# Optimization experiments

Measured on AMD Instinct MI355X. Metric: run time of the kernel, lower is better.

## Reference

```python
import jax, jax.numpy as jnp
import numpy as np
from jax import lax

THRESHOLD = 1.0  # threshold_potential from __init__
STRIDE = (1, 1)
PADDING = 'SAME'


def setup_inputs() -> dict:
    key = jax.random.key(0)
    k1, k2, k3 = jax.random.split(key, 3)
    input_to_layer = jax.random.normal(k1, (1, 512, 512, 16), dtype=jnp.float32)
    weights = jax.random.normal(k2, (3, 3, 16, 64), dtype=jnp.float32)
    old_potentials = jax.random.normal(k3, (1, 512, 512, 64), dtype=jnp.float32)
    return {
        'input_to_layer': input_to_layer,
        'weights': weights,
        'old_potentials': old_potentials,
    }


def reference(input_to_layer, weights, old_potentials):
    # conv2d NHWC x HWIO -> NHWC, SAME padding, stride 1 (as tf.nn.conv2d)
    out_conv = lax.conv_general_dilated(
        input_to_layer, weights,
        window_strides=STRIDE, padding=PADDING,
        dimension_numbers=('NHWC', 'HWIO', 'NHWC'))
    # accumulate membrane potential, fused threshold -> spike + reset
    new_potentials = out_conv + old_potentials
    spiked = new_potentials >= THRESHOLD
    curr_spikes = spiked.astype(new_potentials.dtype)
    new_potentials = jnp.where(spiked, 0.0, new_potentials)
    # original returns spikes; new_potentials is the updated state
    return curr_spikes, new_potentials
```

## Files before the change

kernel.cpp:

```cpp
#include <hip/hip_runtime.h>


#define H 512
#define W 512
#define CI 16
#define CO 64
#define TX 32
#define TY 8
#define XT 34
#define YT 10
#define PIX_US 24
#define KS 152

typedef float v4f __attribute__((ext_vector_type(4)));
typedef float f32x4 __attribute__((ext_vector_type(4)));
typedef short short8 __attribute__((ext_vector_type(8)));
typedef unsigned int uint4v __attribute__((ext_vector_type(4)));

__device__ __forceinline__ unsigned int pack2bf(float f0, float f1) {
    unsigned u0 = __builtin_bit_cast(unsigned, f0);
    unsigned u1 = __builtin_bit_cast(unsigned, f1);
    u0 = (u0 + 0x7FFFu + ((u0 >> 16) & 1u)) >> 16;
    u1 = (u1 + 0x7FFFu + ((u1 >> 16) & 1u)) >> 16;
    return u0 | (u1 << 16);
}

__global__ __launch_bounds__(256, 3)
void snn_conv_mfma(const float* __restrict__ in,
                   const float* __restrict__ w,
                   const float* __restrict__ oldp,
                   float* __restrict__ out_spk,
                   float* __restrict__ out_pot)
{
    __shared__ unsigned short s_in[YT * XT * PIX_US];
    __shared__ unsigned short s_w[CO * KS];

    const int tid = threadIdx.x;
    const int bx = blockIdx.x & 15;
    const int by = blockIdx.x >> 4;
    const int tx0 = bx * TX, ty0 = by * TY;

    {
        const int n  = tid & 63;
        const int kq = tid >> 6;
        #pragma unroll
        for (int kk = 0; kk < 18; ++kk) {
            const int k = kq * 36 + kk * 2;
            const float f0 = w[k * CO + n];
            const float f1 = w[(k + 1) * CO + n];
            *(unsigned int*)&s_w[n * KS + k] = pack2bf(f0, f1);
        }
    }

    for (int idx = tid; idx < YT * XT; idx += 256) {
        const int ly = idx / XT, lx = idx - ly * XT;
        const int gy = ty0 + ly - 1, gx = tx0 + lx - 1;
        uint4v pk0, pk1;
        if ((unsigned)gy < H && (unsigned)gx < W) {
            const v4f* p = (const v4f*)(in + (gy * W + gx) * CI);
            v4f a = p[0], b = p[1], c = p[2], d = p[3];
            pk0 = (uint4v){pack2bf(a.x, a.y), pack2bf(a.z, a.w),
                           pack2bf(b.x, b.y), pack2bf(b.z, b.w)};
            pk1 = (uint4v){pack2bf(c.x, c.y), pack2bf(c.z, c.w),
                           pack2bf(d.x, d.y), pack2bf(d.z, d.w)};
        } else {
            pk0 = (uint4v)0u;
            pk1 = (uint4v)0u;
        }
        uint4v* dst = (uint4v*)&s_in[idx * PIX_US];
        dst[0] = pk0;
        dst[1] = pk1;
    }
    __syncthreads();

    const int lane = tid & 63;
    const int wv   = tid >> 6;
    const int r    = lane & 15;
    const int quad = lane >> 4;
    const int half = quad & 1;
    const int tsel = quad >> 1;

    f32x4 acc[4][4] = {};

    int abase[4];
    #pragma unroll
    for (int mt = 0; mt < 4; ++mt) {
        const int rl = 2 * wv + (mt >> 1);
        const int xl = (mt & 1) * 16 + r;
        abase[mt] = (rl * XT + xl) * PIX_US + half * 8;
    }

    const short8 zero8 = {0, 0, 0, 0, 0, 0, 0, 0};

    #pragma unroll
    for (int ks5 = 0; ks5 < 5; ++ks5) {
        const int t0 = ks5 * 2;
        const int t1 = (ks5 == 4) ? 8 : ks5 * 2 + 1;
        const int off0 = ((t0 / 3) * XT + (t0 % 3)) * PIX_US;
        const int off1 = ((t1 / 3) * XT + (t1 % 3)) * PIX_US;
        const int aoff = tsel ? off1 : off0;
        const int koff = (ks5 < 4) ? (ks5 * 32 + quad * 8) : (128 + half * 8);

        short8 bf[4];
        #pragma unroll
        for (int nt = 0; nt < 4; ++nt)
            bf[nt] = *(const short8*)&s_w[(nt * 16 + r) * KS + koff];

        short8 af[4];
        #pragma unroll
        for (int mt = 0; mt < 4; ++mt) {
            short8 a = *(const short8*)&s_in[abase[mt] + aoff];
            if (ks5 == 4) a = (quad >= 2) ? zero8 : a;
            af[mt] = a;
        }

        #pragma unroll
        for (int mt = 0; mt < 4; ++mt)
            #pragma unroll
            for (int nt = 0; nt < 4; ++nt)
                acc[mt][nt] = __builtin_amdgcn_mfma_f32_16x16x32_bf16(
                    bf[nt], af[mt], acc[mt][nt], 0, 0, 0);
    }

    f32x4 oldv[4][4];
    int ebase[4];
    #pragma unroll
    for (int mt = 0; mt < 4; ++mt) {
        const int gy = ty0 + 2 * wv + (mt >> 1);
        const int gx = tx0 + (mt & 1) * 16 + r;
        ebase[mt] = (gy * W + gx) * CO + quad * 4;
        #pragma unroll
        for (int nt = 0; nt < 4; ++nt)
            oldv[mt][nt] = *(const f32x4*)(oldp + ebase[mt] + nt * 16);
    }

    #pragma unroll
    for (int mt = 0; mt < 4; ++mt) {
        #pragma unroll
        for (int nt = 0; nt < 4; ++nt) {
            const int idx = ebase[mt] + nt * 16;
            f32x4 np = acc[mt][nt] + oldv[mt][nt];
            f32x4 spk, pot;
            #pragma unroll
            for (int j = 0; j < 4; ++j) {
                const bool s = np[j] >= 1.0f;
                spk[j] = s ? 1.0f : 0.0f;
                pot[j] = s ? 0.0f : np[j];
            }
            *(f32x4*)(out_spk + idx) = spk;
            *(f32x4*)(out_pot + idx) = pot;
        }
    }
}

extern "C" void kernel_launch(void* const* d_in, const int* in_sizes, int n_in,
                              void* d_out, int out_size, void* d_ws, size_t ws_size,
                              hipStream_t stream) {
    const float* in   = (const float*)d_in[0];
    const float* w    = (const float*)d_in[1];
    const float* oldp = (const float*)d_in[2];
    float* out_spk = (float*)d_out;
    float* out_pot = out_spk + (size_t)H * W * CO;

    const int grid = (W / TX) * (H / TY);
    snn_conv_mfma<<<grid, 256, 0, stream>>>(in, w, oldp, out_spk, out_pot);
}
```

Measured before the change: 203.7 us.

## Prepack bf16 weights, halve tile height, prefetch old potentials, nontemporal stores

Weight packing to bf16 moves into a separate one-block kernel that writes to workspace, so each conv block just copies pre-packed 16-byte chunks into LDS. The tile height drops from 8 to 4 rows, halving per-wave accumulators and raising the occupancy hint to 4 blocks per CU, at the cost of more halo overhead per output. The old-potential loads are issued at kernel start so they overlap the LDS staging and MFMA work. Output stores become nontemporal to avoid polluting cache with streaming writes. The extra kernel launch adds a small fixed cost.

```diff
diff --git a/kernel.cpp b/kernel.cpp
--- a/kernel.cpp
+++ b/kernel.cpp
@@ -6,11 +6,12 @@
 #define CI 16
 #define CO 64
 #define TX 32
-#define TY 8
+#define TY 4
 #define XT 34
-#define YT 10
+#define YT 6
 #define PIX_US 24
 #define KS 152
+#define SW_CHUNKS ((CO * KS * 2) / 16)
 
 typedef float v4f __attribute__((ext_vector_type(4)));
 typedef float f32x4 __attribute__((ext_vector_type(4)));
@@ -25,35 +26,71 @@
     return u0 | (u1 << 16);
 }
 
-__global__ __launch_bounds__(256, 3)
+__global__ void snn_pack_w(const float* __restrict__ w,
+                           unsigned int* __restrict__ wsu)
+{
+    const int tid = threadIdx.x;
+    const int n  = tid & 63;
+    const int kq = tid >> 6;
+    #pragma unroll
+    for (int kk = 0; kk < 18; ++kk) {
+        const int k = kq * 36 + kk * 2;
+        const float f0 = w[k * CO + n];
+        const float f1 = w[(k + 1) * CO + n];
+        wsu[(n * KS + k) >> 1] = pack2bf(f0, f1);
+    }
+    if (kq == 3) {
+        #pragma unroll
+        for (int i = 0; i < 4; ++i)
+            wsu[((n * KS + 144) >> 1) + i] = 0u;
+    }
+}
+
+__global__ __launch_bounds__(256, 4)
 void snn_conv_mfma(const float* __restrict__ in,
-                   const float* __restrict__ w,
+                   const uint4v* __restrict__ wsv,
                    const float* __restrict__ oldp,
                    float* __restrict__ out_spk,
                    float* __restrict__ out_pot)
 {
     __shared__ unsigned short s_in[YT * XT * PIX_US];
-    __shared__ unsigned short s_w[CO * KS];
+    __shared__ alignas(16) unsigned short s_w[CO * KS];
 
     const int tid = threadIdx.x;
     const int bx = blockIdx.x & 15;
     const int by = blockIdx.x >> 4;
     const int tx0 = bx * TX, ty0 = by * TY;
 
+    const int lane = tid & 63;
+    const int wv   = tid >> 6;
+    const int r    = lane & 15;
+    const int quad = lane >> 4;
+    const int half = quad & 1;
+    const int tsel = quad >> 1;
+
+    f32x4 oldv[2][4];
+    int ebase[2];
+    #pragma unroll
+    for (int mt = 0; mt < 2; ++mt) {
+        const int gy = ty0 + wv;
+        const int gx = tx0 + mt * 16 + r;
+        ebase[mt] = (gy * W + gx) * CO + quad * 4;
+        #pragma unroll
+        for (int nt = 0; nt < 4; ++nt)
+            oldv[mt][nt] = *(const f32x4*)(oldp + ebase[mt] + nt * 16);
+    }
+
     {
-        const int n  = tid & 63;
-        const int kq = tid >> 6;
+        uint4v* dst = (uint4v*)s_w;
         #pragma unroll
-        for (int kk = 0; kk < 18; ++kk) {
-            const int k = kq * 36 + kk * 2;
-            const float f0 = w[k * CO + n];
-            const float f1 = w[(k + 1) * CO + n];
-            *(unsigned int*)&s_w[n * KS + k] = pack2bf(f0, f1);
+        for (int i = 0; i < 5; ++i) {
+            const int idx = tid + i * 256;
+            if (idx < SW_CHUNKS) dst[idx] = wsv[idx];
         }
     }
 
-    for (int idx = tid; idx < YT * XT; idx += 256) {
-        const int ly = idx / XT, lx = idx - ly * XT;
+    if (tid < YT * XT) {
+        const int ly = tid / XT, lx = tid - ly * XT;
         const int gy = ty0 + ly - 1, gx = tx0 + lx - 1;
         uint4v pk0, pk1;
         if ((unsigned)gy < H && (unsigned)gx < W) {
@@ -67,28 +104,18 @@
             pk0 = (uint4v)0u;
             pk1 = (uint4v)0u;
         }
-        uint4v* dst = (uint4v*)&s_in[idx * PIX_US];
+        uint4v* dst = (uint4v*)&s_in[tid * PIX_US];
         dst[0] = pk0;
         dst[1] = pk1;
     }
     __syncthreads();
 
-    const int lane = tid & 63;
-    const int wv   = tid >> 6;
-    const int r    = lane & 15;
-    const int quad = lane >> 4;
-    const int half = quad & 1;
-    const int tsel = quad >> 1;
+    f32x4 acc[2][4] = {};
 
-    f32x4 acc[4][4] = {};
-
-    int abase[4];
+    int abase[2];
     #pragma unroll
-    for (int mt = 0; mt < 4; ++mt) {
-        const int rl = 2 * wv + (mt >> 1);
-        const int xl = (mt & 1) * 16 + r;
-        abase[mt] = (rl * XT + xl) * PIX_US + half * 8;
-    }
+    for (int mt = 0; mt < 2; ++mt)
+        abase[mt] = (wv * XT + mt * 16 + r) * PIX_US + half * 8;
 
     const short8 zero8 = {0, 0, 0, 0, 0, 0, 0, 0};
 
@@ -106,36 +133,24 @@
         for (int nt = 0; nt < 4; ++nt)
             bf[nt] = *(const short8*)&s_w[(nt * 16 + r) * KS + koff];
 
-        short8 af[4];
+        short8 af[2];
         #pragma unroll
-        for (int mt = 0; mt < 4; ++mt) {
+        for (int mt = 0; mt < 2; ++mt) {
             short8 a = *(const short8*)&s_in[abase[mt] + aoff];
             if (ks5 == 4) a = (quad >= 2) ? zero8 : a;
             af[mt] = a;
         }
 
         #pragma unroll
-        for (int mt = 0; mt < 4; ++mt)
+        for (int mt = 0; mt < 2; ++mt)
             #pragma unroll
             for (int nt = 0; nt < 4; ++nt)
                 acc[mt][nt] = __builtin_amdgcn_mfma_f32_16x16x32_bf16(
                     bf[nt], af[mt], acc[mt][nt], 0, 0, 0);
     }
 
-    f32x4 oldv[4][4];
-    int ebase[4];
     #pragma unroll
-    for (int mt = 0; mt < 4; ++mt) {
-        const int gy = ty0 + 2 * wv + (mt >> 1);
-        const int gx = tx0 + (mt & 1) * 16 + r;
-        ebase[mt] = (gy * W + gx) * CO + quad * 4;
-        #pragma unroll
-        for (int nt = 0; nt < 4; ++nt)
-            oldv[mt][nt] = *(const f32x4*)(oldp + ebase[mt] + nt * 16);
-    }
-
-    #pragma unroll
-    for (int mt = 0; mt < 4; ++mt) {
+    for (int mt = 0; mt < 2; ++mt) {
         #pragma unroll
         for (int nt = 0; nt < 4; ++nt) {
             const int idx = ebase[mt] + nt * 16;
@@ -147,8 +162,8 @@
                 spk[j] = s ? 1.0f : 0.0f;
                 pot[j] = s ? 0.0f : np[j];
             }
-            *(f32x4*)(out_spk + idx) = spk;
-            *(f32x4*)(out_pot + idx) = pot;
+            __builtin_nontemporal_store(spk, (f32x4*)(out_spk + idx));
+            __builtin_nontemporal_store(pot, (f32x4*)(out_pot + idx));
         }
     }
 }
@@ -162,6 +177,9 @@
     float* out_spk = (float*)d_out;
     float* out_pot = out_spk + (size_t)H * W * CO;
 
+    snn_pack_w<<<1, 256, 0, stream>>>(w, (unsigned int*)d_ws);
+
     const int grid = (W / TX) * (H / TY);
-    snn_conv_mfma<<<grid, 256, 0, stream>>>(in, w, oldp, out_spk, out_pot);
+    snn_conv_mfma<<<grid, 256, 0, stream>>>(in, (const uint4v*)d_ws, oldp,
+                                            out_spk, out_pot);
 }
```

New measurement: 221.6 us. 1.09x slower.

## Split bf16 pre-conversion into setup kernel and read padded input from global

Applied to the files above, without the earlier changes.

A separate setup kernel converts the input to a zero-padded bf16 image and the weights to packed bf16 in workspace. The conv kernel drops shared memory and syncthreads, reading A and B fragments directly from global/L2 with smaller 16x4 pixel tiles per block and double-buffered weight loads. This removes per-block halo conversion and LDS staging, at the cost of an extra launch, an extra pass writing and reading the padded image, and more redundant global reads of neighbouring pixels and weights.

```diff
diff --git a/kernel.cpp b/kernel.cpp
--- a/kernel.cpp
+++ b/kernel.cpp
@@ -5,12 +5,11 @@
 #define W 512
 #define CI 16
 #define CO 64
-#define TX 32
-#define TY 8
-#define XT 34
-#define YT 10
-#define PIX_US 24
+#define PW 514
+#define PAD_PX (PW * PW)
 #define KS 152
+#define W_OFF_U16 0
+#define IN_OFF_U16 32768
 
 typedef float v4f __attribute__((ext_vector_type(4)));
 typedef float f32x4 __attribute__((ext_vector_type(4)));
@@ -25,22 +24,13 @@
     return u0 | (u1 << 16);
 }
 
-__global__ __launch_bounds__(256, 3)
-void snn_conv_mfma(const float* __restrict__ in,
-                   const float* __restrict__ w,
-                   const float* __restrict__ oldp,
-                   float* __restrict__ out_spk,
-                   float* __restrict__ out_pot)
+__global__ void snn_setup(const float* __restrict__ in,
+                          const float* __restrict__ w,
+                          unsigned short* __restrict__ ws)
 {
-    __shared__ unsigned short s_in[YT * XT * PIX_US];
-    __shared__ unsigned short s_w[CO * KS];
-
     const int tid = threadIdx.x;
-    const int bx = blockIdx.x & 15;
-    const int by = blockIdx.x >> 4;
-    const int tx0 = bx * TX, ty0 = by * TY;
-
-    {
+    if (blockIdx.x == gridDim.x - 1) {
+        unsigned int* wsu = (unsigned int*)(ws + W_OFF_U16);
         const int n  = tid & 63;
         const int kq = tid >> 6;
         #pragma unroll
@@ -48,31 +38,44 @@
             const int k = kq * 36 + kk * 2;
             const float f0 = w[k * CO + n];
             const float f1 = w[(k + 1) * CO + n];
-            *(unsigned int*)&s_w[n * KS + k] = pack2bf(f0, f1);
+            wsu[(n * KS + k) >> 1] = pack2bf(f0, f1);
         }
+        if (kq == 3) {
+            #pragma unroll
+            for (int i = 0; i < 4; ++i)
+                wsu[((n * KS + 144) >> 1) + i] = 0u;
+        }
+        return;
     }
+    const int p = blockIdx.x * 256 + tid;
+    if (p >= PAD_PX) return;
+    const int py = p / PW, px = p - py * PW;
+    uint4v pk0 = (uint4v)0u, pk1 = (uint4v)0u;
+    if (py >= 1 && py <= H && px >= 1 && px <= W) {
+        const v4f* q = (const v4f*)(in + ((py - 1) * W + (px - 1)) * CI);
+        v4f a = q[0], b = q[1], c = q[2], d = q[3];
+        pk0 = (uint4v){pack2bf(a.x, a.y), pack2bf(a.z, a.w),
+                       pack2bf(b.x, b.y), pack2bf(b.z, b.w)};
+        pk1 = (uint4v){pack2bf(c.x, c.y), pack2bf(c.z, c.w),
+                       pack2bf(d.x, d.y), pack2bf(d.z, d.w)};
+    }
+    uint4v* dst = (uint4v*)(ws + IN_OFF_U16 + p * CI);
+    dst[0] = pk0;
+    dst[1] = pk1;
+}
 
-    for (int idx = tid; idx < YT * XT; idx += 256) {
-        const int ly = idx / XT, lx = idx - ly * XT;
-        const int gy = ty0 + ly - 1, gx = tx0 + lx - 1;
-        uint4v pk0, pk1;
-        if ((unsigned)gy < H && (unsigned)gx < W) {
-            const v4f* p = (const v4f*)(in + (gy * W + gx) * CI);
-            v4f a = p[0], b = p[1], c = p[2], d = p[3];
-            pk0 = (uint4v){pack2bf(a.x, a.y), pack2bf(a.z, a.w),
-                           pack2bf(b.x, b.y), pack2bf(b.z, b.w)};
-            pk1 = (uint4v){pack2bf(c.x, c.y), pack2bf(c.z, c.w),
-                           pack2bf(d.x, d.y), pack2bf(d.z, d.w)};
-        } else {
-            pk0 = (uint4v)0u;
-            pk1 = (uint4v)0u;
-        }
-        uint4v* dst = (uint4v*)&s_in[idx * PIX_US];
-        dst[0] = pk0;
-        dst[1] = pk1;
-    }
-    __syncthreads();
+__global__ __launch_bounds__(256, 3)
+void snn_conv_mfma(const unsigned short* __restrict__ ws,
+                   const float* __restrict__ oldp,
+                   float* __restrict__ out_spk,
+                   float* __restrict__ out_pot)
+{
+    const unsigned short* pin = ws + IN_OFF_U16;
+    const unsigned short* wsb = ws + W_OFF_U16;
 
+    const int tid  = threadIdx.x;
+    const int bx   = blockIdx.x & 31;
+    const int by   = blockIdx.x >> 5;
     const int lane = tid & 63;
     const int wv   = tid >> 6;
     const int r    = lane & 15;
@@ -80,76 +83,64 @@
     const int half = quad & 1;
     const int tsel = quad >> 1;
 
-    f32x4 acc[4][4] = {};
+    const int gy = by * 4 + wv;
+    const int gx = bx * 16 + r;
 
-    int abase[4];
+    const int eb = (gy * W + gx) * CO + quad * 4;
+    f32x4 oldv[4];
     #pragma unroll
-    for (int mt = 0; mt < 4; ++mt) {
-        const int rl = 2 * wv + (mt >> 1);
-        const int xl = (mt & 1) * 16 + r;
-        abase[mt] = (rl * XT + xl) * PIX_US + half * 8;
+    for (int nt = 0; nt < 4; ++nt)
+        oldv[nt] = *(const f32x4*)(oldp + eb + nt * 16);
+
+    short8 af[5];
+    #pragma unroll
+    for (int ks5 = 0; ks5 < 5; ++ks5) {
+        const int t = (ks5 == 4) ? 8 : (2 * ks5 + tsel);
+        const int dy = t / 3, dx = t % 3;
+        af[ks5] = *(const short8*)&pin[((gy + dy) * PW + (gx + dx)) * CI + half * 8];
+    }
+    {
+        const short8 zero8 = {0, 0, 0, 0, 0, 0, 0, 0};
+        if (quad >= 2) af[4] = zero8;
     }
 
-    const short8 zero8 = {0, 0, 0, 0, 0, 0, 0, 0};
+    f32x4 acc[4] = {};
+    short8 bf_a[4], bf_b[4];
+
+    #pragma unroll
+    for (int nt = 0; nt < 4; ++nt)
+        bf_a[nt] = *(const short8*)&wsb[(nt * 16 + r) * KS + quad * 8];
 
     #pragma unroll
     for (int ks5 = 0; ks5 < 5; ++ks5) {
-        const int t0 = ks5 * 2;
-        const int t1 = (ks5 == 4) ? 8 : ks5 * 2 + 1;
-        const int off0 = ((t0 / 3) * XT + (t0 % 3)) * PIX_US;
-        const int off1 = ((t1 / 3) * XT + (t1 % 3)) * PIX_US;
-        const int aoff = tsel ? off1 : off0;
-        const int koff = (ks5 < 4) ? (ks5 * 32 + quad * 8) : (128 + half * 8);
-
-        short8 bf[4];
+        short8* cur = (ks5 & 1) ? bf_b : bf_a;
+        short8* nxt = (ks5 & 1) ? bf_a : bf_b;
+        if (ks5 < 4) {
+            const int koff = (ks5 == 3) ? (128 + half * 8)
+                                        : ((ks5 + 1) * 32 + quad * 8);
+            #pragma unroll
+            for (int nt = 0; nt < 4; ++nt)
+                nxt[nt] = *(const short8*)&wsb[(nt * 16 + r) * KS + koff];
+        }
         #pragma unroll
         for (int nt = 0; nt < 4; ++nt)
-            bf[nt] = *(const short8*)&s_w[(nt * 16 + r) * KS + koff];
-
-        short8 af[4];
-        #pragma unroll
-        for (int mt = 0; mt < 4; ++mt) {
-            short8 a = *(const short8*)&s_in[abase[mt] + aoff];
-            if (ks5 == 4) a = (quad >= 2) ? zero8 : a;
-            af[mt] = a;
-        }
-
-        #pragma unroll
-        for (int mt = 0; mt < 4; ++mt)
-            #pragma unroll
-            for (int nt = 0; nt < 4; ++nt)
-                acc[mt][nt] = __builtin_amdgcn_mfma_f32_16x16x32_bf16(
-                    bf[nt], af[mt], acc[mt][nt], 0, 0, 0);
-    }
-
-    f32x4 oldv[4][4];
-    int ebase[4];
-    #pragma unroll
-    for (int mt = 0; mt < 4; ++mt) {
-        const int gy = ty0 + 2 * wv + (mt >> 1);
-        const int gx = tx0 + (mt & 1) * 16 + r;
-        ebase[mt] = (gy * W + gx) * CO + quad * 4;
-        #pragma unroll
-        for (int nt = 0; nt < 4; ++nt)
-            oldv[mt][nt] = *(const f32x4*)(oldp + ebase[mt] + nt * 16);
+            acc[nt] = __builtin_amdgcn_mfma_f32_16x16x32_bf16(
+                cur[nt], af[ks5], acc[nt], 0, 0, 0);
     }
 
     #pragma unroll
-    for (int mt = 0; mt < 4; ++mt) {
+    for (int nt = 0; nt < 4; ++nt) {
+        const int idx = eb + nt * 16;
+        f32x4 np = acc[nt] + oldv[nt];
+        f32x4 spk, pot;
         #pragma unroll
-        for (int nt = 0; nt < 4; ++nt) {
-            const int idx = ebase[mt] + nt * 16;
-            f32x4 np = acc[mt][nt] + oldv[mt][nt];
-            f32x4 spk, pot;
-            #pragma unroll
-            for (int j = 0; j < 4; ++j) {
-                const bool s = np[j] >= 1.0f;
-                spk[j] = s ? 1.0f : 0.0f;
-                pot[j] = s ? 0.0f : np[j];
-            }
-            *(f32x4*)(out_spk + idx) = spk;
-            *(f32x4*)(out_pot + idx) = pot;
+        for (int j = 0; j < 4; ++j) {
+            const bool s = np[j] >= 1.0f;
+            spk[j] = s ? 1.0f : 0.0f;
+            pot[j] = s ? 0.0f : np[j];
         }
+        *(f32x4*)(out_spk + idx) = spk;
+        *(f32x4*)(out_pot + idx) = pot;
     }
 }
 
@@ -161,7 +152,11 @@
     const float* oldp = (const float*)d_in[2];
     float* out_spk = (float*)d_out;
     float* out_pot = out_spk + (size_t)H * W * CO;
+    unsigned short* ws = (unsigned short*)d_ws;
 
-    const int grid = (W / TX) * (H / TY);
-    snn_conv_mfma<<<grid, 256, 0, stream>>>(in, w, oldp, out_spk, out_pot);
+    const int setup_grid = (PAD_PX + 255) / 256 + 1;
+    snn_setup<<<setup_grid, 256, 0, stream>>>(in, w, ws);
+
+    const int grid = (W / 16) * (H / 4);
+    snn_conv_mfma<<<grid, 256, 0, stream>>>(ws, oldp, out_spk, out_pot);
 }
```

Result: slower. 222.3 us (+9.1%).
